# Kernel tuning notes

Hardware: AMD Instinct MI355X
Metric: run time of the kernel (lower is better)

## Reference

```python
import jax, jax.numpy as jnp
import numpy as np

PI = 3.14159  # constant as written in the source
V = 10        # node count hard-coded by the module


def setup_inputs() -> dict:
    key = jax.random.key(0)
    ks = jax.random.split(key, 10)
    B, T, F = 128, 200, 256
    end_output = jax.random.normal(ks[0], (B, T, V, F), dtype=jnp.float32)
    S = jax.random.uniform(ks[1], (B, T, V, V), dtype=jnp.float32)  # values in [0,1)
    mul = jax.random.normal(ks[2], (V, V), dtype=jnp.float32) * 0.05
    bias = jax.random.normal(ks[3], (V, V), dtype=jnp.float32) * 0.05
    means = jax.random.normal(ks[4], (1, V), dtype=jnp.float32) * 0.05
    stds = 0.5 + jax.random.uniform(ks[5], (1, V), dtype=jnp.float32)  # keep away from 0
    emb_in = jax.random.normal(ks[6], (F, F), dtype=jnp.float32) * 0.05
    emb_out = jax.random.normal(ks[7], (F, F), dtype=jnp.float32) * 0.05
    emb3 = jax.random.normal(ks[8], (V, V), dtype=jnp.float32) * 0.05
    emb4 = jax.random.normal(ks[9], (V, V), dtype=jnp.float32) * 0.05
    return {"end_output": end_output, "S": S, "mul": mul, "bias": bias,
            "means": means, "stds": stds, "emb_in": emb_in, "emb_out": emb_out,
            "emb3": emb3, "emb4": emb4}


def reference(end_output, S, mul, bias, means, stds, emb_in, emb_out, emb3, emb4):
    # end_output: (B,T,V,F), S: (B,T,V,V)
    S = jnp.minimum(S, jnp.swapaxes(S, -1, -2))  # symmetrize

    # GaussianLayer: K.dot(S, mul) + bias, gaussian pdf, sigmoid, then tanh
    x = jnp.einsum('btij,jk->btik', S, mul) + bias
    a = (2.0 * PI) ** 0.5
    tmp = jnp.exp(-0.5 * ((x - means) / stds) ** 2) / (a * stds)
    edge_feature = jnp.tanh(jax.nn.sigmoid(tmp))  # (B,T,V,V)

    # Degree (centrality) embedding: D = K.sum(A, axis=1) -> sum over rows
    D = jnp.sum(S, axis=-2)  # (B,T,V)
    Di = jax.lax.stop_gradient(D).astype(jnp.int32)
    outputs = end_output + emb_in[Di] + emb_out[Di]  # (B,T,V,F)

    # Floyd-Warshall APSP, vectorized over (B,T); accumulate update-indicator * edge_feature
    dist = S
    sp = jnp.zeros_like(S)
    for k in range(V):
        temp = dist[..., :, k:k + 1] + dist[..., k:k + 1, :]  # dist[i,k] + dist[k,j]
        new = jnp.minimum(dist, temp)
        upd = (new != dist).astype(dist.dtype)  # 1 where relaxed
        sp = sp + upd * edge_feature
        dist = new

    Spatial_i = jax.lax.stop_gradient(dist).astype(jnp.int32)  # (B,T,V,V) in [0,V)
    Edge_i = jax.lax.stop_gradient(sp).astype(jnp.int32)       # (B,T,V,V) in [0,V)
    Spatial_Encoding = jnp.sum(emb3[Spatial_i], axis=-2)  # (B,T,V,10)
    Edge_Encoding = jnp.sum(emb4[Edge_i], axis=-2)         # (B,T,V,10)
    atten_bias = Edge_Encoding + Spatial_Encoding
    return outputs, atten_bias
```

## Files before the change

kernel.cpp:

```cpp
#include <hip/hip_runtime.h>
#include <math.h>

constexpr int NV = 10;
constexpr int NF = 256;

__global__ __launch_bounds__(256) void graph_emb_kernel(
    const float* __restrict__ end_output,
    const float* __restrict__ S,
    const float* __restrict__ mul,
    const float* __restrict__ bias,
    const float* __restrict__ means,
    const float* __restrict__ stds,
    const float* __restrict__ emb_in,
    const float* __restrict__ emb_out,
    const float* __restrict__ emb3,
    const float* __restrict__ emb4,
    float* __restrict__ out_main,
    float* __restrict__ out_atten)
{
    __shared__ __attribute__((aligned(16))) float s_embsum[NV * NF];
    __shared__ float s_mul[NV * NV];
    __shared__ float s_bias[NV * NV];
    __shared__ float s_means[NV];
    __shared__ float s_stds[NV];
    __shared__ float s_emb3[NV * NV];
    __shared__ float s_emb4[NV * NV];
    __shared__ float s_sym[NV * NV];
    __shared__ float s_ef[NV * NV];
    __shared__ float s_dist[NV * NV];
    __shared__ float s_sp[NV * NV];
    __shared__ int   s_si[NV * NV];
    __shared__ int   s_ei[NV * NV];
    __shared__ int   s_Di[NV];

    const int tid = threadIdx.x;
    const int bt  = blockIdx.x;
    const size_t slab = (size_t)bt * (NV * NF);
    const int g0 = bt * (NV * NV);

    #pragma unroll
    for (int k = 0; k < NV; ++k) {
        int idx = k * 256 + tid;
        s_embsum[idx] = emb_in[idx] + emb_out[idx];
    }
    if (tid < NV * NV) {
        s_mul[tid]  = mul[tid];
        s_bias[tid] = bias[tid];
        s_emb3[tid] = emb3[tid];
        s_emb4[tid] = emb4[tid];
        int i = tid / NV, j = tid % NV;
        float a = S[g0 + tid];
        float b = S[g0 + j * NV + i];
        s_sym[tid] = fminf(a, b);
    }
    if (tid >= 128 && tid < 128 + NV) {
        s_means[tid - 128] = means[tid - 128];
        s_stds[tid - 128]  = stds[tid - 128];
    }
    __syncthreads();

    if (tid < NV * NV) {
        int i = tid / NV, c = tid % NV;
        float acc = 0.f;
        #pragma unroll
        for (int j = 0; j < NV; ++j)
            acc += s_sym[i * NV + j] * s_mul[j * NV + c];
        float x = acc + s_bias[tid];
        const float A = sqrtf(2.0f * 3.14159f);
        float z = (x - s_means[c]) / s_stds[c];
        float tmp = expf(-0.5f * z * z) / (A * s_stds[c]);
        float sg = 1.0f / (1.0f + expf(-tmp));
        s_ef[tid]   = tanhf(sg);
        s_dist[tid] = s_sym[tid];
        s_sp[tid]   = 0.f;
    }
    if (tid >= 128 && tid < 128 + NV) {
        int c = tid - 128;
        float d = 0.f;
        #pragma unroll
        for (int i = 0; i < NV; ++i) d += s_sym[i * NV + c];
        int di = (int)d;
        s_Di[c] = min(max(di, 0), NV - 1);
    }
    __syncthreads();

    #pragma unroll
    for (int k = 0; k < NV; ++k) {
        if (tid < NV * NV) {
            int i = tid / NV, j = tid % NV;
            float t = s_dist[i * NV + k] + s_dist[k * NV + j];
            if (t < s_dist[tid]) {
                s_dist[tid] = t;
                s_sp[tid] += s_ef[tid];
            }
        }
        __syncthreads();
    }

    if (tid < NV * NV) {
        int si = (int)s_dist[tid];
        int ei = (int)s_sp[tid];
        s_si[tid] = min(max(si, 0), NV - 1);
        s_ei[tid] = min(max(ei, 0), NV - 1);
    }
    __syncthreads();

    if (tid < NV * NV) {
        int i = tid / NV, c = tid % NV;
        float acc3 = 0.f, acc4 = 0.f;
        #pragma unroll
        for (int j = 0; j < NV; ++j) {
            acc3 += s_emb3[s_si[i * NV + j] * NV + c];
            acc4 += s_emb4[s_ei[i * NV + j] * NV + c];
        }
        out_atten[g0 + tid] = acc4 + acc3;
    }

    const float4* end4 = reinterpret_cast<const float4*>(end_output + slab);
    float4*       out4 = reinterpret_cast<float4*>(out_main + slab);
    const float4* es4  = reinterpret_cast<const float4*>(s_embsum);
    for (int u = tid; u < NV * NF / 4; u += 256) {
        int row = u >> 6;
        int f4  = u & 63;
        float4 e = end4[u];
        float4 s = es4[s_Di[row] * (NF / 4) + f4];
        e.x += s.x; e.y += s.y; e.z += s.z; e.w += s.w;
        out4[u] = e;
    }
}

extern "C" void kernel_launch(void* const* d_in, const int* in_sizes, int n_in,
                              void* d_out, int out_size, void* d_ws, size_t ws_size,
                              hipStream_t stream) {
    const float* end_output = (const float*)d_in[0];
    const float* S          = (const float*)d_in[1];
    const float* mul        = (const float*)d_in[2];
    const float* bias       = (const float*)d_in[3];
    const float* means      = (const float*)d_in[4];
    const float* stds       = (const float*)d_in[5];
    const float* emb_in     = (const float*)d_in[6];
    const float* emb_out    = (const float*)d_in[7];
    const float* emb3       = (const float*)d_in[8];
    const float* emb4       = (const float*)d_in[9];

    float* out_main  = (float*)d_out;
    float* out_atten = out_main + (size_t)in_sizes[0];

    const int BT = in_sizes[1] / (NV * NV);

    graph_emb_kernel<<<BT, 256, 0, stream>>>(
        end_output, S, mul, bias, means, stds,
        emb_in, emb_out, emb3, emb4, out_main, out_atten);
}
```

Before: 479.2 us.

## Process four graphs per block with one wave per graph, dropping block barriers

Each 256-thread block now handles four (b,t) graphs, giving each wavefront one graph. Each lane owns up to two of its graph's 100 cells, so Floyd-Warshall runs within a single wave and needs no __syncthreads between steps. This spreads the emb_in+emb_out table load into shared memory over four graphs, and the block's barriers are cut to two. The risk is that the per-wave work serializes two cells per lane and depends on lockstep wave execution for the shared-memory dist updates.

```diff
diff --git a/kernel.cpp b/kernel.cpp
--- a/kernel.cpp
+++ b/kernel.cpp
@@ -1,10 +1,12 @@
 #include <hip/hip_runtime.h>
 #include <math.h>
 
-constexpr int NV = 10;
-constexpr int NF = 256;
+constexpr int NV  = 10;
+constexpr int NF  = 256;
+constexpr int NC  = NV * NV;
+constexpr int GPB = 4;
 
-__global__ __launch_bounds__(256) void graph_emb_kernel(
+__global__ __launch_bounds__(256) void graph_emb_fused(
     const float* __restrict__ end_output,
     const float* __restrict__ S,
     const float* __restrict__ mul,
@@ -16,42 +18,30 @@
     const float* __restrict__ emb3,
     const float* __restrict__ emb4,
     float* __restrict__ out_main,
-    float* __restrict__ out_atten)
+    float* __restrict__ out_atten,
+    int BT)
 {
     __shared__ __attribute__((aligned(16))) float s_embsum[NV * NF];
-    __shared__ float s_mul[NV * NV];
-    __shared__ float s_bias[NV * NV];
-    __shared__ float s_means[NV];
-    __shared__ float s_stds[NV];
-    __shared__ float s_emb3[NV * NV];
-    __shared__ float s_emb4[NV * NV];
-    __shared__ float s_sym[NV * NV];
-    __shared__ float s_ef[NV * NV];
-    __shared__ float s_dist[NV * NV];
-    __shared__ float s_sp[NV * NV];
-    __shared__ int   s_si[NV * NV];
-    __shared__ int   s_ei[NV * NV];
-    __shared__ int   s_Di[NV];
+    __shared__ float s_mul[NC], s_bias[NC], s_emb3[NC], s_emb4[NC];
+    __shared__ float s_means[NV], s_stds[NV];
+    __shared__ float s_dist[GPB][NC];
+    __shared__ int   s_si[GPB][NC];
+    __shared__ int   s_ei[GPB][NC];
+    __shared__ int   s_Di[GPB][NV];
 
-    const int tid = threadIdx.x;
-    const int bt  = blockIdx.x;
-    const size_t slab = (size_t)bt * (NV * NF);
-    const int g0 = bt * (NV * NV);
+    const int tid  = threadIdx.x;
+    const int wave = tid >> 6;
+    const int lane = tid & 63;
+    const int gbase = blockIdx.x * GPB;
+    const int g     = gbase + wave;
 
-    #pragma unroll
-    for (int k = 0; k < NV; ++k) {
-        int idx = k * 256 + tid;
+    for (int idx = tid; idx < NV * NF; idx += 256)
         s_embsum[idx] = emb_in[idx] + emb_out[idx];
-    }
-    if (tid < NV * NV) {
+    if (tid < NC) {
         s_mul[tid]  = mul[tid];
         s_bias[tid] = bias[tid];
         s_emb3[tid] = emb3[tid];
         s_emb4[tid] = emb4[tid];
-        int i = tid / NV, j = tid % NV;
-        float a = S[g0 + tid];
-        float b = S[g0 + j * NV + i];
-        s_sym[tid] = fminf(a, b);
     }
     if (tid >= 128 && tid < 128 + NV) {
         s_means[tid - 128] = means[tid - 128];
@@ -59,71 +49,110 @@
     }
     __syncthreads();
 
-    if (tid < NV * NV) {
-        int i = tid / NV, c = tid % NV;
-        float acc = 0.f;
+    if (g < BT) {
+        const int g0 = g * NC;
+        const int c0 = lane;
+        const int c1 = 64 + lane;
+        const bool has1 = (lane < 36);
+        const int i0 = c0 / NV, j0 = c0 % NV;
+        const int i1 = c1 / NV, j1 = c1 % NV;
+
+        s_dist[wave][c0] = fminf(S[g0 + c0], S[g0 + j0 * NV + i0]);
+        if (has1)
+            s_dist[wave][c1] = fminf(S[g0 + c1], S[g0 + j1 * NV + i1]);
+
+        const float A = sqrtf(2.0f * 3.14159f);
+        float ef0 = 0.f, ef1 = 0.f, sp0 = 0.f, sp1 = 0.f;
+        {
+            float acc = 0.f;
+            #pragma unroll
+            for (int j = 0; j < NV; ++j)
+                acc += s_dist[wave][i0 * NV + j] * s_mul[j * NV + j0];
+            float x = acc + s_bias[c0];
+            float z = (x - s_means[j0]) / s_stds[j0];
+            float tmp = expf(-0.5f * z * z) / (A * s_stds[j0]);
+            float sg = 1.0f / (1.0f + expf(-tmp));
+            ef0 = tanhf(sg);
+        }
+        if (has1) {
+            float acc = 0.f;
+            #pragma unroll
+            for (int j = 0; j < NV; ++j)
+                acc += s_dist[wave][i1 * NV + j] * s_mul[j * NV + j1];
+            float x = acc + s_bias[c1];
+            float z = (x - s_means[j1]) / s_stds[j1];
+            float tmp = expf(-0.5f * z * z) / (A * s_stds[j1]);
+            float sg = 1.0f / (1.0f + expf(-tmp));
+            ef1 = tanhf(sg);
+        }
+
+        if (lane < NV) {
+            float d = 0.f;
+            #pragma unroll
+            for (int i = 0; i < NV; ++i) d += s_dist[wave][i * NV + lane];
+            int di = (int)d;
+            s_Di[wave][lane] = min(max(di, 0), NV - 1);
+        }
+
         #pragma unroll
-        for (int j = 0; j < NV; ++j)
-            acc += s_sym[i * NV + j] * s_mul[j * NV + c];
-        float x = acc + s_bias[tid];
-        const float A = sqrtf(2.0f * 3.14159f);
-        float z = (x - s_means[c]) / s_stds[c];
-        float tmp = expf(-0.5f * z * z) / (A * s_stds[c]);
-        float sg = 1.0f / (1.0f + expf(-tmp));
-        s_ef[tid]   = tanhf(sg);
-        s_dist[tid] = s_sym[tid];
-        s_sp[tid]   = 0.f;
+        for (int k = 0; k < NV; ++k) {
+            float t0 = s_dist[wave][i0 * NV + k] + s_dist[wave][k * NV + j0];
+            if (t0 < s_dist[wave][c0]) { s_dist[wave][c0] = t0; sp0 += ef0; }
+            if (has1) {
+                float t1 = s_dist[wave][i1 * NV + k] + s_dist[wave][k * NV + j1];
+                if (t1 < s_dist[wave][c1]) { s_dist[wave][c1] = t1; sp1 += ef1; }
+            }
+        }
+
+        {
+            int si = (int)s_dist[wave][c0];
+            int ei = (int)sp0;
+            s_si[wave][c0] = min(max(si, 0), NV - 1);
+            s_ei[wave][c0] = min(max(ei, 0), NV - 1);
+        }
+        if (has1) {
+            int si = (int)s_dist[wave][c1];
+            int ei = (int)sp1;
+            s_si[wave][c1] = min(max(si, 0), NV - 1);
+            s_ei[wave][c1] = min(max(ei, 0), NV - 1);
+        }
+
+        {
+            float acc3 = 0.f, acc4 = 0.f;
+            #pragma unroll
+            for (int j = 0; j < NV; ++j) {
+                acc3 += s_emb3[s_si[wave][i0 * NV + j] * NV + j0];
+                acc4 += s_emb4[s_ei[wave][i0 * NV + j] * NV + j0];
+            }
+            out_atten[g0 + c0] = acc4 + acc3;
+        }
+        if (has1) {
+            float acc3 = 0.f, acc4 = 0.f;
+            #pragma unroll
+            for (int j = 0; j < NV; ++j) {
+                acc3 += s_emb3[s_si[wave][i1 * NV + j] * NV + j1];
+                acc4 += s_emb4[s_ei[wave][i1 * NV + j] * NV + j1];
+            }
+            out_atten[g0 + c1] = acc4 + acc3;
+        }
     }
-    if (tid >= 128 && tid < 128 + NV) {
-        int c = tid - 128;
-        float d = 0.f;
-        #pragma unroll
-        for (int i = 0; i < NV; ++i) d += s_sym[i * NV + c];
-        int di = (int)d;
-        s_Di[c] = min(max(di, 0), NV - 1);
-    }
+
     __syncthreads();
 
-    #pragma unroll
-    for (int k = 0; k < NV; ++k) {
-        if (tid < NV * NV) {
-            int i = tid / NV, j = tid % NV;
-            float t = s_dist[i * NV + k] + s_dist[k * NV + j];
-            if (t < s_dist[tid]) {
-                s_dist[tid] = t;
-                s_sp[tid] += s_ef[tid];
-            }
-        }
-        __syncthreads();
-    }
-
-    if (tid < NV * NV) {
-        int si = (int)s_dist[tid];
-        int ei = (int)s_sp[tid];
-        s_si[tid] = min(max(si, 0), NV - 1);
-        s_ei[tid] = min(max(ei, 0), NV - 1);
-    }
-    __syncthreads();
-
-    if (tid < NV * NV) {
-        int i = tid / NV, c = tid % NV;
-        float acc3 = 0.f, acc4 = 0.f;
-        #pragma unroll
-        for (int j = 0; j < NV; ++j) {
-            acc3 += s_emb3[s_si[i * NV + j] * NV + c];
-            acc4 += s_emb4[s_ei[i * NV + j] * NV + c];
-        }
-        out_atten[g0 + tid] = acc4 + acc3;
-    }
-
+    const int ng = min(GPB, BT - gbase);
+    const size_t slab = (size_t)gbase * (NV * NF);
     const float4* end4 = reinterpret_cast<const float4*>(end_output + slab);
     float4*       out4 = reinterpret_cast<float4*>(out_main + slab);
     const float4* es4  = reinterpret_cast<const float4*>(s_embsum);
-    for (int u = tid; u < NV * NF / 4; u += 256) {
-        int row = u >> 6;
-        int f4  = u & 63;
+    const int items = ng * (NV * NF / 4);
+
+    for (int u = tid; u < items; u += 256) {
+        int gg  = u / 640;
+        int rem = u - gg * 640;
+        int row = rem >> 6;
+        int f4  = rem & 63;
         float4 e = end4[u];
-        float4 s = es4[s_Di[row] * (NF / 4) + f4];
+        float4 s = es4[s_Di[gg][row] * (NF / 4) + f4];
         e.x += s.x; e.y += s.y; e.z += s.z; e.w += s.w;
         out4[u] = e;
     }
@@ -147,8 +176,9 @@
     float* out_atten = out_main + (size_t)in_sizes[0];
 
     const int BT = in_sizes[1] / (NV * NV);
+    const int nblocks = (BT + GPB - 1) / GPB;
 
-    graph_emb_kernel<<<BT, 256, 0, stream>>>(
+    graph_emb_fused<<<nblocks, 256, 0, stream>>>(
         end_output, S, mul, bias, means, stds,
-        emb_in, emb_out, emb3, emb4, out_main, out_atten);
+        emb_in, emb_out, emb3, emb4, out_main, out_atten, BT);
 }
```

Result: faster. 464.4 us (-3.1%).
